# Performance work log

Hardware: AMD Instinct MI355X
Metric: run time of the kernel (lower is better)

Reference implementation:

```python
import jax, jax.numpy as jnp
import numpy as np

N_TERMS = 20  # matches n_terms=20 default in the torch series expansion


def lower_reg_inc_gamma_series(alpha, x):
    # prefactor = x**alpha * exp(-x)   (1-D x branch of the torch code)
    prefactor = x ** alpha * jnp.exp(-x)
    # denominator_i = alpha * (alpha+1) * ... * (alpha+i), i = 0..N_TERMS-1
    js = jnp.arange(1, N_TERMS, dtype=x.dtype)
    denom = alpha * jnp.concatenate([jnp.ones((1,), x.dtype), jnp.cumprod(alpha + js)])  # [N_TERMS]
    i = jnp.arange(N_TERMS, dtype=x.dtype)
    # sum_i x^i / denom_i  -> [N, N_TERMS] intermediate, reduced over terms
    sum_of_terms = jnp.sum(x[..., None] ** i / denom, axis=-1)
    return prefactor * sum_of_terms / jnp.exp(jax.lax.lgamma(alpha))


def setup_inputs() -> dict:
    key = jax.random.key(0)
    k1, k2, k3, k4 = jax.random.split(key, 4)
    N, T = 1_000_000, 50
    # strictly positive times so log()/pow() are well-defined
    deltas = jax.random.uniform(k1, (N, 1), jnp.float32, 0.01, 0.5)
    event_times = jax.random.uniform(k2, (N,), jnp.float32, 0.5, 5.0)
    cov_times = jax.random.uniform(k3, (N, T), jnp.float32, 0.01, 3.0)
    censoring_indicators = jax.random.bernoulli(k4, 0.3, (N,))
    global_theta = jnp.array([2.0, 1.5], dtype=jnp.float32)  # (alpha, beta)
    return {
        "deltas": deltas,
        "event_times": event_times,
        "cov_times": cov_times,
        "censoring_indicators": censoring_indicators,
        "global_theta": global_theta,
    }


def reference(deltas, event_times, cov_times, censoring_indicators, global_theta):
    alpha = global_theta[0]
    beta = global_theta[1]
    d = deltas[:, 0]  # squeeze(1)
    shifted_event_times = event_times + d
    shifted_cov_times = jnp.max(cov_times, axis=1) + d

    # Gamma(alpha, rate=beta) log pdf
    logpdf = (alpha * jnp.log(beta) - jax.lax.lgamma(alpha)
              + (alpha - 1.0) * jnp.log(shifted_event_times)
              - beta * shifted_event_times)

    # "logsurv" as written in the source: 1 - P(alpha, beta*t) (series estimate)
    logsurv = 1.0 - lower_reg_inc_gamma_series(alpha, shifted_event_times * beta)
    lognormalization = 1.0 - lower_reg_inc_gamma_series(alpha, shifted_cov_times * beta)

    logprob = jnp.where(censoring_indicators, logsurv, logpdf) - lognormalization
    return jnp.mean(logprob)
```

## Files before the change

### kernel.cpp

```cpp
#include <hip/hip_runtime.h>
#include <math.h>

#define NTERMS 20
#define ROWS_PER_BLOCK 256
#define BLOCK 256

__device__ __forceinline__ float lower_reg_inc_gamma(float a, float x, float inv_gamma_a) {
    float term = 1.0f / a;
    float sum  = term;
    #pragma unroll
    for (int i = 1; i < NTERMS; ++i) {
        term *= x / (a + (float)i);
        sum  += term;
    }
    return powf(x, a) * expf(-x) * sum * inv_gamma_a;
}

__global__ __launch_bounds__(BLOCK) void gamma_logprob_main(
    const float* __restrict__ deltas,
    const float* __restrict__ event_times,
    const float* __restrict__ cov_times,
    const int*   __restrict__ cens,
    const float* __restrict__ theta,
    double*      __restrict__ partials,
    int N, int T)
{
    __shared__ float covbuf[ROWS_PER_BLOCK * 50];
    __shared__ double sdata[BLOCK / 64];

    const int tid   = threadIdx.x;
    const int rows0 = blockIdx.x * ROWS_PER_BLOCK;
    const int nrows = min(ROWS_PER_BLOCK, N - rows0);

    {
        const float2* gsrc = reinterpret_cast<const float2*>(cov_times + (size_t)rows0 * T);
        float2* lbuf = reinterpret_cast<float2*>(covbuf);
        const int nf2 = (nrows * T) >> 1;
        for (int i = tid; i < nf2; i += BLOCK)
            lbuf[i] = gsrc[i];
        if ((nrows * T) & 1) {
            if (tid == 0)
                covbuf[nrows * T - 1] = cov_times[(size_t)rows0 * T + nrows * T - 1];
        }
    }
    __syncthreads();

    const float alpha     = theta[0];
    const float beta      = theta[1];
    const float lgam      = lgammaf(alpha);
    const float inv_gamma = expf(-lgam);
    const float a_log_b   = alpha * logf(beta);

    double acc = 0.0;
    if (tid < nrows) {
        const int row   = rows0 + tid;
        const float d   = deltas[row];
        const float set = event_times[row] + d;

        const float2* lp = reinterpret_cast<const float2*>(covbuf + tid * T);
        float m = -INFINITY;
        const int T2 = T >> 1;
        #pragma unroll 5
        for (int j = 0; j < T2; ++j) {
            float2 v = lp[j];
            m = fmaxf(m, fmaxf(v.x, v.y));
        }
        if (T & 1) m = fmaxf(m, covbuf[tid * T + T - 1]);
        const float sct = m + d;

        const float logpdf  = a_log_b - lgam + (alpha - 1.0f) * logf(set) - beta * set;
        const float logsurv = 1.0f - lower_reg_inc_gamma(alpha, set * beta, inv_gamma);
        const float lognorm = 1.0f - lower_reg_inc_gamma(alpha, sct * beta, inv_gamma);

        const float lp_ = (cens[row] != 0 ? logsurv : logpdf) - lognorm;
        acc = (double)lp_;
    }

    #pragma unroll
    for (int off = 32; off > 0; off >>= 1)
        acc += __shfl_down(acc, off, 64);

    const int lane = tid & 63;
    const int wid  = tid >> 6;
    if (lane == 0) sdata[wid] = acc;
    __syncthreads();
    if (tid == 0) {
        double s = 0.0;
        #pragma unroll
        for (int w = 0; w < BLOCK / 64; ++w) s += sdata[w];
        partials[blockIdx.x] = s;
    }
}

__global__ __launch_bounds__(256) void gamma_logprob_finalize(
    const double* __restrict__ partials, int nblocks,
    float* __restrict__ out, double invN)
{
    double acc = 0.0;
    for (int i = threadIdx.x; i < nblocks; i += 256)
        acc += partials[i];

    #pragma unroll
    for (int off = 32; off > 0; off >>= 1)
        acc += __shfl_down(acc, off, 64);

    __shared__ double sdata[4];
    const int lane = threadIdx.x & 63;
    const int wid  = threadIdx.x >> 6;
    if (lane == 0) sdata[wid] = acc;
    __syncthreads();
    if (threadIdx.x == 0) {
        double s = sdata[0] + sdata[1] + sdata[2] + sdata[3];
        out[0] = (float)(s * invN);
    }
}

extern "C" void kernel_launch(void* const* d_in, const int* in_sizes, int n_in,
                              void* d_out, int out_size, void* d_ws, size_t ws_size,
                              hipStream_t stream) {
    const float* deltas      = (const float*)d_in[0];
    const float* event_times = (const float*)d_in[1];
    const float* cov_times   = (const float*)d_in[2];
    const int*   cens        = (const int*)d_in[3];
    const float* theta       = (const float*)d_in[4];
    float* out = (float*)d_out;

    const int N = in_sizes[1];
    const int T = in_sizes[2] / N;

    double* partials = (double*)d_ws;

    const int grid = (N + ROWS_PER_BLOCK - 1) / ROWS_PER_BLOCK;

    gamma_logprob_main<<<grid, BLOCK, 0, stream>>>(
        deltas, event_times, cov_times, cens, theta, partials, N, T);
    gamma_logprob_finalize<<<1, 256, 0, stream>>>(
        partials, grid, out, 1.0 / (double)N);
}
```

Baseline: 341.3 us.

## Compute row max via 8-lane shuffle groups, drop LDS staging, precompute series coefficients

Replaces the 51 KB shared-memory staging of cov_times with direct global loads, where groups of 8 lanes each reduce one row's max using xor shuffles. The smaller LDS footprint allows more blocks per CU. A tiny setup kernel precomputes the 20 series coefficients, folding in 1/Gamma(alpha), plus the logpdf constants, so the main kernel evaluates the sum as a Horner polynomial. The power term is also computed as a single exp of alpha*log(x)-x. This adds an extra kernel launch and changes the summation order, and the strided 8-lane loads may coalesce less well than the float2 copy.

```diff
diff --git a/kernel.cpp b/kernel.cpp
--- a/kernel.cpp
+++ b/kernel.cpp
@@ -2,18 +2,26 @@
 #include <math.h>
 
 #define NTERMS 20
+#define BLOCK 256
 #define ROWS_PER_BLOCK 256
-#define BLOCK 256
 
-__device__ __forceinline__ float lower_reg_inc_gamma(float a, float x, float inv_gamma_a) {
-    float term = 1.0f / a;
-    float sum  = term;
-    #pragma unroll
+#define WS_PARTIALS_OFF 1024
+
+__global__ void gamma_setup(const float* __restrict__ theta, float* __restrict__ ws) {
+    const float a  = theta[0];
+    const float b  = theta[1];
+    const float lg = lgammaf(a);
+    const float inv_g = expf(-lg);
+    float c = inv_g / a;
+    ws[0] = c;
     for (int i = 1; i < NTERMS; ++i) {
-        term *= x / (a + (float)i);
-        sum  += term;
+        c = c / (a + (float)i);
+        ws[i] = c;
     }
-    return powf(x, a) * expf(-x) * sum * inv_gamma_a;
+    ws[20] = a * logf(b) - lg;
+    ws[21] = logf(b);
+    ws[22] = a;
+    ws[23] = b;
 }
 
 __global__ __launch_bounds__(BLOCK) void gamma_logprob_main(
@@ -21,59 +29,76 @@
     const float* __restrict__ event_times,
     const float* __restrict__ cov_times,
     const int*   __restrict__ cens,
-    const float* __restrict__ theta,
+    const float* __restrict__ ws,
     double*      __restrict__ partials,
     int N, int T)
 {
-    __shared__ float covbuf[ROWS_PER_BLOCK * 50];
+    __shared__ float  lmax[ROWS_PER_BLOCK];
     __shared__ double sdata[BLOCK / 64];
 
     const int tid   = threadIdx.x;
     const int rows0 = blockIdx.x * ROWS_PER_BLOCK;
     const int nrows = min(ROWS_PER_BLOCK, N - rows0);
 
-    {
-        const float2* gsrc = reinterpret_cast<const float2*>(cov_times + (size_t)rows0 * T);
-        float2* lbuf = reinterpret_cast<float2*>(covbuf);
-        const int nf2 = (nrows * T) >> 1;
-        for (int i = tid; i < nf2; i += BLOCK)
-            lbuf[i] = gsrc[i];
-        if ((nrows * T) & 1) {
-            if (tid == 0)
-                covbuf[nrows * T - 1] = cov_times[(size_t)rows0 * T + nrows * T - 1];
+    const int g = tid >> 3;
+    const int k = tid & 7;
+    #pragma unroll
+    for (int p = 0; p < ROWS_PER_BLOCK / 32; ++p) {
+        const int prow = p * 32 + g;
+        if (prow < nrows) {
+            const float* rp = cov_times + (size_t)(rows0 + prow) * T;
+            float m = -INFINITY;
+            #pragma unroll
+            for (int j = 0; j < 7; ++j) {
+                const int idx = k + 8 * j;
+                if (idx < T) m = fmaxf(m, rp[idx]);
+            }
+            m = fmaxf(m, __shfl_xor(m, 1, 64));
+            m = fmaxf(m, __shfl_xor(m, 2, 64));
+            m = fmaxf(m, __shfl_xor(m, 4, 64));
+            if (k == 0) lmax[prow] = m;
         }
     }
+
+    float c[NTERMS];
+    #pragma unroll
+    for (int i = 0; i < NTERMS; ++i) c[i] = ws[i];
+    const float C1    = ws[20];
+    const float logb  = ws[21];
+    const float alpha = ws[22];
+    const float beta  = ws[23];
+
     __syncthreads();
-
-    const float alpha     = theta[0];
-    const float beta      = theta[1];
-    const float lgam      = lgammaf(alpha);
-    const float inv_gamma = expf(-lgam);
-    const float a_log_b   = alpha * logf(beta);
 
     double acc = 0.0;
     if (tid < nrows) {
         const int row   = rows0 + tid;
         const float d   = deltas[row];
         const float set = event_times[row] + d;
+        const float sct = lmax[tid] + d;
 
-        const float2* lp = reinterpret_cast<const float2*>(covbuf + tid * T);
-        float m = -INFINITY;
-        const int T2 = T >> 1;
-        #pragma unroll 5
-        for (int j = 0; j < T2; ++j) {
-            float2 v = lp[j];
-            m = fmaxf(m, fmaxf(v.x, v.y));
+        const float x1 = set * beta;
+        const float x2 = sct * beta;
+
+        const float lnset = logf(set);
+        const float lx1   = lnset + logb;
+        const float lx2   = logf(x2);
+
+        float s1 = c[NTERMS - 1], s2 = c[NTERMS - 1];
+        #pragma unroll
+        for (int i = NTERMS - 2; i >= 0; --i) {
+            s1 = fmaf(s1, x1, c[i]);
+            s2 = fmaf(s2, x2, c[i]);
         }
-        if (T & 1) m = fmaxf(m, covbuf[tid * T + T - 1]);
-        const float sct = m + d;
+        const float P1 = expf(fmaf(alpha, lx1, -x1)) * s1;
+        const float P2 = expf(fmaf(alpha, lx2, -x2)) * s2;
 
-        const float logpdf  = a_log_b - lgam + (alpha - 1.0f) * logf(set) - beta * set;
-        const float logsurv = 1.0f - lower_reg_inc_gamma(alpha, set * beta, inv_gamma);
-        const float lognorm = 1.0f - lower_reg_inc_gamma(alpha, sct * beta, inv_gamma);
+        const float logpdf  = C1 + (alpha - 1.0f) * lnset - beta * set;
+        const float logsurv = 1.0f - P1;
+        const float lognorm = 1.0f - P2;
 
-        const float lp_ = (cens[row] != 0 ? logsurv : logpdf) - lognorm;
-        acc = (double)lp_;
+        const float lp = (cens[row] != 0 ? logsurv : logpdf) - lognorm;
+        acc = (double)lp;
     }
 
     #pragma unroll
@@ -128,12 +153,16 @@
     const int N = in_sizes[1];
     const int T = in_sizes[2] / N;
 
-    double* partials = (double*)d_ws;
+    float*  wsf      = (float*)d_ws;
+    double* partials = (double*)((char*)d_ws + WS_PARTIALS_OFF);
 
     const int grid = (N + ROWS_PER_BLOCK - 1) / ROWS_PER_BLOCK;
 
+    gamma_setup<<<1, 1, 0, stream>>>((const float*)d_in[4], wsf);
     gamma_logprob_main<<<grid, BLOCK, 0, stream>>>(
-        deltas, event_times, cov_times, cens, theta, partials, N, T);
+        deltas, event_times, cov_times, cens, wsf, partials, N, T);
     gamma_logprob_finalize<<<1, 256, 0, stream>>>(
         partials, grid, out, 1.0 / (double)N);
+
+    (void)theta; (void)n_in; (void)out_size; (void)ws_size;
 }
```

Measured after the change: 323.0 us. 1.06x faster.
